# Kernel tuning notes

Hardware: AMD Instinct MI355X
Metric: run time of the kernel (lower is better)

Reference implementation:

```python
import jax, jax.numpy as jnp
import numpy as np

NUM_HEADS = 16

def setup_inputs() -> dict:
    key = jax.random.key(0)
    ks = jax.random.split(key, 8)
    T, B, E = 2048, 2, 1024
    s = 1.0 / np.sqrt(E)
    return {
        "query": jax.random.normal(ks[0], (T, B, E), jnp.float32),
        "key": jax.random.normal(ks[1], (T, B, E), jnp.float32),
        "value": jax.random.normal(ks[2], (T, B, E), jnp.float32),
        "Wq": jax.random.normal(ks[3], (E, E), jnp.float32) * s,
        "bq": jnp.zeros((E,), jnp.float32),
        "Wk": jax.random.normal(ks[4], (E, E), jnp.float32) * s,
        "bk": jnp.zeros((E,), jnp.float32),
        "Wv": jax.random.normal(ks[5], (E, E), jnp.float32) * s,
        "bv": jnp.zeros((E,), jnp.float32),
        "Wo": jax.random.normal(ks[6], (E, E), jnp.float32) * s,
        "bo": jnp.zeros((E,), jnp.float32),
    }

def reference(query, key, value, Wq, bq, Wk, bk, Wv, bv, Wo, bo):
    T, B, E = query.shape
    S = key.shape[0]
    H = NUM_HEADS
    hd = E // H
    scaling = float(hd) ** -0.5
    # linear projections (torch Linear: x @ W.T + b)
    q = (query @ Wq.T + bq).reshape(T, B, H, hd)
    k = (key @ Wk.T + bk).reshape(S, B, H, hd)
    v = (value @ Wv.T + bv).reshape(S, B, H, hd)
    # scores: (B, H, T, S)
    scores = jnp.einsum('tbhd,sbhd->bhts', q, k) * scaling
    attn = jax.nn.softmax(scores, axis=-1)  # dropout p=0
    # weighted sum: (T, B, H, hd) -> (T, B, E)
    out = jnp.einsum('bhts,sbhd->tbhd', attn, v).reshape(T, B, E)
    out = out @ Wo.T + bo
    # averaged attention weights over heads: (B, T, S)
    avg_w = attn.mean(axis=1)
    return (out, avg_w)
```

## Files before the change

### kernel.cpp

```cpp
#include <hip/hip_runtime.h>
#include <hip/hip_bf16.h>
#include <stdint.h>

#define HN 16
#define TT 2048
#define BBATCH 2
#define EE 1024
#define HD 64
#define MM 4096

typedef __attribute__((ext_vector_type(8))) __bf16 bfrag;
typedef __attribute__((ext_vector_type(4))) float f32x4;

__device__ __forceinline__ void gll16(const void* g, void* lds) {
  __builtin_amdgcn_global_load_lds(
      (const __attribute__((address_space(1))) void*)g,
      (__attribute__((address_space(3))) void*)lds, 16, 0, 0);
}

__device__ __forceinline__ f32x4 mfma_bf16(bfrag a, bfrag b, f32x4 c) {
  return __builtin_amdgcn_mfma_f32_16x16x32_bf16(a, b, c, 0, 0, 0);
}

__device__ __forceinline__ const bfrag* fragp(const __bf16* base, int row, int e) {
  return (const bfrag*)(base + row * 64 + ((((e >> 3) ^ row) & 7) << 3));
}
__device__ __forceinline__ int swze(int row, int col) {
  return row * 64 + ((((col >> 3) ^ row) & 7) << 3) + (col & 7);
}
__device__ __forceinline__ void stage8(const __bf16* grow0, int gstride,
                                       __bf16* tile, int r0, int lane) {
  const int rr = lane >> 3;
  const int cl = (lane & 7) ^ rr;
  gll16(grow0 + (size_t)(r0 + rr) * gstride + cl * 8, tile + r0 * 64);
}

struct CvtArgs {
  const float* src[7];
  __bf16* dst[7];
  int n4[7];
};

__global__ __launch_bounds__(256) void cvt_all(CvtArgs a) {
  const int z = blockIdx.z;
  const int i = blockIdx.x * 256 + threadIdx.x;
  if (i < a.n4[z]) {
    float4 v = ((const float4*)a.src[z])[i];
    struct alignas(8) B4 { __bf16 a0, a1, a2, a3; };
    B4 o = {(__bf16)v.x, (__bf16)v.y, (__bf16)v.z, (__bf16)v.w};
    ((B4*)a.dst[z])[i] = o;
  }
}

__device__ __forceinline__ void gemm_core(const __bf16* __restrict__ X,
                                          const __bf16* __restrict__ W,
                                          const float* __restrict__ bias,
                                          void* __restrict__ out, int mode) {
  __shared__ __bf16 As[128 * 32];
  __shared__ __bf16 Bs[128 * 32];
  const int tid = threadIdx.x;
  const int lane = tid & 63, wave = tid >> 6;
  const int wm = wave >> 1, wn = wave & 1;
  const int quad = lane >> 4, l16 = lane & 15;
  const int m0 = blockIdx.y * 128, n0 = blockIdx.x * 128;
  const int srow = lane >> 2;
  const int scol = (lane & 3) * 8;
  const int c0 = 2 * wave;

  f32x4 acc[4][4] = {};

  for (int k0 = 0; k0 < EE; k0 += 32) {
    #pragma unroll
    for (int c = 0; c < 2; ++c) {
      const int ch = c0 + c;
      gll16(X + (size_t)(m0 + ch * 16 + srow) * EE + k0 + scol, As + ch * 512);
      gll16(W + (size_t)(n0 + ch * 16 + srow) * EE + k0 + scol, Bs + ch * 512);
    }
    __syncthreads();
    bfrag a[4], b[4];
    #pragma unroll
    for (int f = 0; f < 4; ++f)
      a[f] = *(const bfrag*)(As + (wm * 64 + f * 16 + l16) * 32 + quad * 8);
    #pragma unroll
    for (int f = 0; f < 4; ++f)
      b[f] = *(const bfrag*)(Bs + (wn * 64 + f * 16 + l16) * 32 + quad * 8);
    #pragma unroll
    for (int fm = 0; fm < 4; ++fm)
      #pragma unroll
      for (int fn = 0; fn < 4; ++fn)
        acc[fm][fn] = mfma_bf16(a[fm], b[fn], acc[fm][fn]);
    __syncthreads();
  }

  float bv[4];
  #pragma unroll
  for (int fn = 0; fn < 4; ++fn) bv[fn] = bias[n0 + wn * 64 + fn * 16 + l16];

  #pragma unroll
  for (int fm = 0; fm < 4; ++fm) {
    #pragma unroll
    for (int r = 0; r < 4; ++r) {
      const int gm = m0 + wm * 64 + fm * 16 + quad * 4 + r;
      #pragma unroll
      for (int fn = 0; fn < 4; ++fn) {
        const int gn = n0 + wn * 64 + fn * 16 + l16;
        const float v = acc[fm][fn][r] + bv[fn];
        if (mode == 0) {
          const int t = gm >> 1, bb = gm & 1, h = gn >> 6, d = gn & 63;
          ((__bf16*)out)[(((size_t)(bb * HN + h)) * TT + t) * HD + d] = (__bf16)v;
        } else {
          const int s = gm >> 1, bb = gm & 1, h = gn >> 6, d = gn & 63;
          ((__bf16*)out)[(((size_t)(bb * HN + h)) * HD + d) * TT + s] = (__bf16)v;
        }
      }
    }
  }
}

__global__ __launch_bounds__(256) void gemm_qkv(
    const __bf16* __restrict__ xq, const __bf16* __restrict__ xk,
    const __bf16* __restrict__ xv, const __bf16* __restrict__ wq,
    const __bf16* __restrict__ wk, const __bf16* __restrict__ wv,
    const float* __restrict__ bq, const float* __restrict__ bk,
    const float* __restrict__ bv, __bf16* __restrict__ qo,
    __bf16* __restrict__ ko, __bf16* __restrict__ vo) {
  const __bf16 *X, *W;
  const float* bias;
  __bf16* out;
  int mode;
  if (blockIdx.z == 0)      { X = xq; W = wq; bias = bq; out = qo; mode = 0; }
  else if (blockIdx.z == 1) { X = xk; W = wk; bias = bk; out = ko; mode = 0; }
  else                      { X = xv; W = wv; bias = bv; out = vo; mode = 2; }
  gemm_core(X, W, bias, out, mode);
}

__global__ __launch_bounds__(256) void gemm_o64(const __bf16* __restrict__ X,
                                                const __bf16* __restrict__ W,
                                                const float* __restrict__ bias,
                                                float* __restrict__ out) {
  __shared__ __bf16 As[64 * 32];
  __shared__ __bf16 Bs[128 * 32];
  const int tid = threadIdx.x;
  const int lane = tid & 63, wave = tid >> 6;
  const int quad = lane >> 4, l16 = lane & 15;
  const int m0 = blockIdx.y * 64, n0 = blockIdx.x * 128;
  const int srow = lane >> 2, scol = (lane & 3) * 8;

  f32x4 acc[4][2] = {};

  for (int k0 = 0; k0 < EE; k0 += 32) {
    gll16(X + (size_t)(m0 + wave * 16 + srow) * EE + k0 + scol, As + wave * 512);
    #pragma unroll
    for (int c = 0; c < 2; ++c) {
      const int ch = 2 * wave + c;
      gll16(W + (size_t)(n0 + ch * 16 + srow) * EE + k0 + scol, Bs + ch * 512);
    }
    __syncthreads();
    bfrag a[4], b2[2];
    #pragma unroll
    for (int f = 0; f < 4; ++f)
      a[f] = *(const bfrag*)(As + (f * 16 + l16) * 32 + quad * 8);
    #pragma unroll
    for (int f = 0; f < 2; ++f)
      b2[f] = *(const bfrag*)(Bs + (wave * 32 + f * 16 + l16) * 32 + quad * 8);
    #pragma unroll
    for (int fm = 0; fm < 4; ++fm)
      #pragma unroll
      for (int fn = 0; fn < 2; ++fn)
        acc[fm][fn] = mfma_bf16(a[fm], b2[fn], acc[fm][fn]);
    __syncthreads();
  }

  float bv[2];
  #pragma unroll
  for (int fn = 0; fn < 2; ++fn) bv[fn] = bias[n0 + wave * 32 + fn * 16 + l16];

  #pragma unroll
  for (int fm = 0; fm < 4; ++fm)
    #pragma unroll
    for (int r = 0; r < 4; ++r) {
      const int gm = m0 + fm * 16 + quad * 4 + r;
      #pragma unroll
      for (int fn = 0; fn < 2; ++fn) {
        const int gn = n0 + wave * 32 + fn * 16 + l16;
        out[(size_t)gm * EE + gn] = acc[fm][fn][r] + bv[fn];
      }
    }
}

__global__ __launch_bounds__(256) void attn_fwd(const __bf16* __restrict__ qb,
                                                const __bf16* __restrict__ kb,
                                                const __bf16* __restrict__ vtb,
                                                __bf16* __restrict__ ob,
                                                float* __restrict__ linv_ws) {
  __shared__ __bf16 QP[128 * 64];
  __shared__ __bf16 Ks[2][64 * 64];
  __shared__ __bf16 Vs[2][64 * 64];

  const int tid = threadIdx.x, lane = tid & 63, w = tid >> 6;
  const int quad = lane >> 4, l16 = lane & 15;
  const int t0 = blockIdx.x * 128;
  const int h = blockIdx.y, b = blockIdx.z;
  const size_t bh = (size_t)(b * HN + h);

  const __bf16* qbase = qb + (bh * TT + t0) * HD;
  const __bf16* kbase = kb + bh * TT * HD;
  const __bf16* vbase = vtb + bh * HD * TT;

  #pragma unroll
  for (int c = 0; c < 4; ++c) stage8(qbase, HD, QP, w * 32 + c * 8, lane);
  #pragma unroll
  for (int c = 0; c < 2; ++c) {
    stage8(kbase, HD, Ks[0], w * 16 + c * 8, lane);
    stage8(vbase + 0, TT, Vs[0], w * 16 + c * 8, lane);
  }
  __syncthreads();

  bfrag qf[2][2];
  #pragma unroll
  for (int f = 0; f < 2; ++f)
    #pragma unroll
    for (int ks = 0; ks < 2; ++ks)
      qf[f][ks] = *fragp(QP, w * 32 + f * 16 + l16, ks * 32 + quad * 8);

  f32x4 oacc[2][4] = {};
  float lpart[2][4] = {};

  for (int it = 0; it < TT / 64; ++it) {
    const int cur = it & 1;
    if (it) __syncthreads();
    if (it + 1 < TT / 64) {
      const int s1 = (it + 1) * 64;
      #pragma unroll
      for (int c = 0; c < 2; ++c) {
        stage8(kbase + (size_t)s1 * HD, HD, Ks[1 - cur], w * 16 + c * 8, lane);
        stage8(vbase + s1, TT, Vs[1 - cur], w * 16 + c * 8, lane);
      }
    }

    f32x4 sacc[2][4] = {};
    #pragma unroll
    for (int ks = 0; ks < 2; ++ks) {
      bfrag kf[4];
      #pragma unroll
      for (int fn = 0; fn < 4; ++fn)
        kf[fn] = *fragp(Ks[cur], fn * 16 + l16, ks * 32 + quad * 8);
      #pragma unroll
      for (int fm = 0; fm < 2; ++fm)
        #pragma unroll
        for (int fn = 0; fn < 4; ++fn)
          sacc[fm][fn] = mfma_bf16(qf[fm][ks], kf[fn], sacc[fm][fn]);
    }

    #pragma unroll
    for (int fm = 0; fm < 2; ++fm)
      #pragma unroll
      for (int fn = 0; fn < 4; ++fn)
        #pragma unroll
        for (int r = 0; r < 4; ++r) {
          const float p = __expf(sacc[fm][fn][r] * 0.125f);
          lpart[fm][r] += p;
          QP[swze(w * 32 + fm * 16 + quad * 4 + r, fn * 16 + l16)] = (__bf16)p;
        }

    #pragma unroll
    for (int ks = 0; ks < 2; ++ks) {
      bfrag pf[2], vf[4];
      #pragma unroll
      for (int fm = 0; fm < 2; ++fm)
        pf[fm] = *fragp(QP, w * 32 + fm * 16 + l16, ks * 32 + quad * 8);
      #pragma unroll
      for (int fn = 0; fn < 4; ++fn)
        vf[fn] = *fragp(Vs[cur], fn * 16 + l16, ks * 32 + quad * 8);
      #pragma unroll
      for (int fm = 0; fm < 2; ++fm)
        #pragma unroll
        for (int fn = 0; fn < 4; ++fn)
          oacc[fm][fn] = mfma_bf16(pf[fm], vf[fn], oacc[fm][fn]);
    }
  }

  float linvv[2][4];
  #pragma unroll
  for (int fm = 0; fm < 2; ++fm)
    #pragma unroll
    for (int r = 0; r < 4; ++r) {
      float v = lpart[fm][r];
      v += __shfl_xor(v, 1, 16);
      v += __shfl_xor(v, 2, 16);
      v += __shfl_xor(v, 4, 16);
      v += __shfl_xor(v, 8, 16);
      linvv[fm][r] = 1.0f / v;
    }
  if (l16 == 0) {
    #pragma unroll
    for (int fm = 0; fm < 2; ++fm)
      #pragma unroll
      for (int r = 0; r < 4; ++r)
        linv_ws[bh * TT + t0 + w * 32 + fm * 16 + quad * 4 + r] = linvv[fm][r];
  }

  #pragma unroll
  for (int fm = 0; fm < 2; ++fm)
    #pragma unroll
    for (int r = 0; r < 4; ++r) {
      const int row = w * 32 + fm * 16 + quad * 4 + r;
      #pragma unroll
      for (int fn = 0; fn < 4; ++fn) {
        const int d = fn * 16 + l16;
        ob[((size_t)(t0 + row) * BBATCH + b) * EE + h * HD + d] =
            (__bf16)(oacc[fm][fn][r] * linvv[fm][r]);
      }
    }
}

__global__ __launch_bounds__(256) void avg_attn(const __bf16* __restrict__ qb,
                                                const __bf16* __restrict__ kb,
                                                const float* __restrict__ linv_ws,
                                                float* __restrict__ avg_out) {
  __shared__ __bf16 Qs[2][128 * 64];
  __shared__ __bf16 Ks2[2][64 * 64];

  const int tid = threadIdx.x, lane = tid & 63, w = tid >> 6;
  const int quad = lane >> 4, l16 = lane & 15;
  const int s0 = blockIdx.x * 64, t0 = blockIdx.y * 128;
  const int b = blockIdx.z;

  {
    const size_t bh0 = (size_t)b * HN;
    #pragma unroll
    for (int c = 0; c < 4; ++c)
      stage8(qb + (bh0 * TT + t0) * HD, HD, Qs[0], w * 32 + c * 8, lane);
    #pragma unroll
    for (int c = 0; c < 2; ++c)
      stage8(kb + (bh0 * TT + s0) * HD, HD, Ks2[0], w * 16 + c * 8, lane);
  }

  f32x4 aacc[2][4] = {};

  for (int h = 0; h < HN; ++h) {
    const int cur = h & 1;
    const size_t bh = (size_t)(b * HN + h);
    __syncthreads();
    if (h + 1 < HN) {
      const size_t bh1 = bh + 1;
      #pragma unroll
      for (int c = 0; c < 4; ++c)
        stage8(qb + (bh1 * TT + t0) * HD, HD, Qs[1 - cur], w * 32 + c * 8, lane);
      #pragma unroll
      for (int c = 0; c < 2; ++c)
        stage8(kb + (bh1 * TT + s0) * HD, HD, Ks2[1 - cur], w * 16 + c * 8, lane);
    }

    f32x4 sacc[2][4] = {};
    #pragma unroll
    for (int ks = 0; ks < 2; ++ks) {
      bfrag qf[2], kf[4];
      #pragma unroll
      for (int fm = 0; fm < 2; ++fm)
        qf[fm] = *fragp(Qs[cur], w * 32 + fm * 16 + l16, ks * 32 + quad * 8);
      #pragma unroll
      for (int fn = 0; fn < 4; ++fn)
        kf[fn] = *fragp(Ks2[cur], fn * 16 + l16, ks * 32 + quad * 8);
      #pragma unroll
      for (int fm = 0; fm < 2; ++fm)
        #pragma unroll
        for (int fn = 0; fn < 4; ++fn)
          sacc[fm][fn] = mfma_bf16(qf[fm], kf[fn], sacc[fm][fn]);
    }

    float lv[2][4];
    #pragma unroll
    for (int fm = 0; fm < 2; ++fm)
      #pragma unroll
      for (int r = 0; r < 4; ++r)
        lv[fm][r] = linv_ws[bh * TT + t0 + w * 32 + fm * 16 + quad * 4 + r];

    #pragma unroll
    for (int fm = 0; fm < 2; ++fm)
      #pragma unroll
      for (int fn = 0; fn < 4; ++fn)
        #pragma unroll
        for (int r = 0; r < 4; ++r)
          aacc[fm][fn][r] += __expf(sacc[fm][fn][r] * 0.125f) * lv[fm][r];
  }

  const float invh = 1.0f / (float)HN;
  #pragma unroll
  for (int fm = 0; fm < 2; ++fm)
    #pragma unroll
    for (int r = 0; r < 4; ++r) {
      const int t = t0 + w * 32 + fm * 16 + quad * 4 + r;
      #pragma unroll
      for (int fn = 0; fn < 4; ++fn) {
        const int s = s0 + fn * 16 + l16;
        avg_out[((size_t)b * TT + t) * TT + s] = aacc[fm][fn][r] * invh;
      }
    }
}

extern "C" void kernel_launch(void* const* d_in, const int* in_sizes, int n_in,
                              void* d_out, int out_size, void* d_ws, size_t ws_size,
                              hipStream_t stream) {
  (void)in_sizes; (void)n_in; (void)out_size; (void)ws_size;
  const float* query = (const float*)d_in[0];
  const float* key   = (const float*)d_in[1];
  const float* value = (const float*)d_in[2];
  const float* Wq = (const float*)d_in[3];
  const float* bq = (const float*)d_in[4];
  const float* Wk = (const float*)d_in[5];
  const float* bk = (const float*)d_in[6];
  const float* Wv = (const float*)d_in[7];
  const float* bv = (const float*)d_in[8];
  const float* Wo = (const float*)d_in[9];
  const float* bo = (const float*)d_in[10];

  char* ws = (char*)d_ws;
  size_t off = 0;
  auto wsalloc = [&](size_t bytes) -> void* {
    void* p = ws + off;
    off += (bytes + 255) & ~(size_t)255;
    return p;
  };
  const size_t XE = (size_t)MM * EE;
  const size_t WE = (size_t)EE * EE;
  __bf16* xq   = (__bf16*)wsalloc(XE * 2);
  __bf16* xk   = (__bf16*)wsalloc(XE * 2);
  __bf16* xv   = (__bf16*)wsalloc(XE * 2);
  __bf16* wqb  = (__bf16*)wsalloc(WE * 2);
  __bf16* wkb  = (__bf16*)wsalloc(WE * 2);
  __bf16* wvb  = (__bf16*)wsalloc(WE * 2);
  __bf16* wob  = (__bf16*)wsalloc(WE * 2);
  __bf16* qbuf = (__bf16*)wsalloc(XE * 2);
  __bf16* kbuf = (__bf16*)wsalloc(XE * 2);
  __bf16* vtbuf= (__bf16*)wsalloc(XE * 2);
  __bf16* obuf = (__bf16*)wsalloc(XE * 2);
  float* linv  = (float*)wsalloc((size_t)BBATCH * HN * TT * 4);

  CvtArgs ca;
  ca.src[0] = query; ca.dst[0] = xq;  ca.n4[0] = (int)(XE / 4);
  ca.src[1] = key;   ca.dst[1] = xk;  ca.n4[1] = (int)(XE / 4);
  ca.src[2] = value; ca.dst[2] = xv;  ca.n4[2] = (int)(XE / 4);
  ca.src[3] = Wq;    ca.dst[3] = wqb; ca.n4[3] = (int)(WE / 4);
  ca.src[4] = Wk;    ca.dst[4] = wkb; ca.n4[4] = (int)(WE / 4);
  ca.src[5] = Wv;    ca.dst[5] = wvb; ca.n4[5] = (int)(WE / 4);
  ca.src[6] = Wo;    ca.dst[6] = wob; ca.n4[6] = (int)(WE / 4);
  cvt_all<<<dim3(4096, 1, 7), 256, 0, stream>>>(ca);

  gemm_qkv<<<dim3(8, 32, 3), 256, 0, stream>>>(xq, xk, xv, wqb, wkb, wvb,
                                               bq, bk, bv, qbuf, kbuf, vtbuf);

  attn_fwd<<<dim3(16, HN, BBATCH), 256, 0, stream>>>(qbuf, kbuf, vtbuf, obuf, linv);

  float* avg_out = (float*)d_out + (size_t)TT * BBATCH * EE;
  avg_attn<<<dim3(32, 16, 2), 256, 0, stream>>>(qbuf, kbuf, linv, avg_out);

  gemm_o64<<<dim3(8, 64), 256, 0, stream>>>(obuf, wob, bo, (float*)d_out);
}
```

Measured before the change: 300.4 us.

## Use 2-wave blocks with 64-row wave tiles and transposed S=K·Q softmax in attention

Attention and averaged-weights kernels now launch 128 threads, and each wave handles 64 query rows instead of 32, doubling the MFMA work per wave and the reuse of loaded K/V fragments. In attn_fwd the score MFMA is transposed to K·Q, so each lane owns a query row. This lets the row sum be reduced with two shuffles and lets P be written to LDS as packed 4-element bf16 stores. avg_attn loads the per-row inverse sums as vectors. The larger register tiles may raise VGPR pressure, and the 512-block grids have half as many waves, which may lower occupancy.

```diff
diff --git a/kernel.cpp b/kernel.cpp
--- a/kernel.cpp
+++ b/kernel.cpp
@@ -24,9 +24,6 @@
 
 __device__ __forceinline__ const bfrag* fragp(const __bf16* base, int row, int e) {
   return (const bfrag*)(base + row * 64 + ((((e >> 3) ^ row) & 7) << 3));
-}
-__device__ __forceinline__ int swze(int row, int col) {
-  return row * 64 + ((((col >> 3) ^ row) & 7) << 3) + (col & 7);
 }
 __device__ __forceinline__ void stage8(const __bf16* grow0, int gstride,
                                        __bf16* tile, int r0, int lane) {
@@ -188,7 +185,7 @@
     }
 }
 
-__global__ __launch_bounds__(256) void attn_fwd(const __bf16* __restrict__ qb,
+__global__ __launch_bounds__(128) void attn_fwd(const __bf16* __restrict__ qb,
                                                 const __bf16* __restrict__ kb,
                                                 const __bf16* __restrict__ vtb,
                                                 __bf16* __restrict__ ob,
@@ -196,6 +193,7 @@
   __shared__ __bf16 QP[128 * 64];
   __shared__ __bf16 Ks[2][64 * 64];
   __shared__ __bf16 Vs[2][64 * 64];
+  __shared__ float LinvS[128];
 
   const int tid = threadIdx.x, lane = tid & 63, w = tid >> 6;
   const int quad = lane >> 4, l16 = lane & 15;
@@ -208,23 +206,23 @@
   const __bf16* vbase = vtb + bh * HD * TT;
 
   #pragma unroll
-  for (int c = 0; c < 4; ++c) stage8(qbase, HD, QP, w * 32 + c * 8, lane);
-  #pragma unroll
-  for (int c = 0; c < 2; ++c) {
-    stage8(kbase, HD, Ks[0], w * 16 + c * 8, lane);
-    stage8(vbase + 0, TT, Vs[0], w * 16 + c * 8, lane);
+  for (int c = 0; c < 8; ++c) stage8(qbase, HD, QP, w * 64 + c * 8, lane);
+  #pragma unroll
+  for (int c = 0; c < 4; ++c) {
+    stage8(kbase, HD, Ks[0], w * 32 + c * 8, lane);
+    stage8(vbase, TT, Vs[0], w * 32 + c * 8, lane);
   }
   __syncthreads();
 
-  bfrag qf[2][2];
-  #pragma unroll
-  for (int f = 0; f < 2; ++f)
+  bfrag qf[4][2];
+  #pragma unroll
+  for (int fn = 0; fn < 4; ++fn)
     #pragma unroll
     for (int ks = 0; ks < 2; ++ks)
-      qf[f][ks] = *fragp(QP, w * 32 + f * 16 + l16, ks * 32 + quad * 8);
-
-  f32x4 oacc[2][4] = {};
-  float lpart[2][4] = {};
+      qf[fn][ks] = *fragp(QP, w * 64 + fn * 16 + l16, ks * 32 + quad * 8);
+
+  f32x4 oacc[4][4] = {};
+  float lpart[4] = {};
 
   for (int it = 0; it < TT / 64; ++it) {
     const int cur = it & 1;
@@ -232,89 +230,90 @@
     if (it + 1 < TT / 64) {
       const int s1 = (it + 1) * 64;
       #pragma unroll
-      for (int c = 0; c < 2; ++c) {
-        stage8(kbase + (size_t)s1 * HD, HD, Ks[1 - cur], w * 16 + c * 8, lane);
-        stage8(vbase + s1, TT, Vs[1 - cur], w * 16 + c * 8, lane);
-      }
-    }
-
-    f32x4 sacc[2][4] = {};
+      for (int c = 0; c < 4; ++c) {
+        stage8(kbase + (size_t)s1 * HD, HD, Ks[1 - cur], w * 32 + c * 8, lane);
+        stage8(vbase + s1, TT, Vs[1 - cur], w * 32 + c * 8, lane);
+      }
+    }
+
+    f32x4 sacc[4][4] = {};
     #pragma unroll
     for (int ks = 0; ks < 2; ++ks) {
       bfrag kf[4];
       #pragma unroll
-      for (int fn = 0; fn < 4; ++fn)
-        kf[fn] = *fragp(Ks[cur], fn * 16 + l16, ks * 32 + quad * 8);
-      #pragma unroll
-      for (int fm = 0; fm < 2; ++fm)
+      for (int f = 0; f < 4; ++f)
+        kf[f] = *fragp(Ks[cur], f * 16 + l16, ks * 32 + quad * 8);
+      #pragma unroll
+      for (int fm = 0; fm < 4; ++fm)
         #pragma unroll
         for (int fn = 0; fn < 4; ++fn)
-          sacc[fm][fn] = mfma_bf16(qf[fm][ks], kf[fn], sacc[fm][fn]);
-    }
-
-    #pragma unroll
-    for (int fm = 0; fm < 2; ++fm)
-      #pragma unroll
-      for (int fn = 0; fn < 4; ++fn)
-        #pragma unroll
-        for (int r = 0; r < 4; ++r) {
-          const float p = __expf(sacc[fm][fn][r] * 0.125f);
-          lpart[fm][r] += p;
-          QP[swze(w * 32 + fm * 16 + quad * 4 + r, fn * 16 + l16)] = (__bf16)p;
-        }
+          sacc[fm][fn] = mfma_bf16(kf[fm], qf[fn][ks], sacc[fm][fn]);
+    }
+
+    #pragma unroll
+    for (int fn = 0; fn < 4; ++fn) {
+      const int row = w * 64 + fn * 16 + l16;
+      float acc_l = 0.0f;
+      #pragma unroll
+      for (int fm = 0; fm < 4; ++fm) {
+        float p0 = __expf(sacc[fm][fn][0] * 0.125f);
+        float p1 = __expf(sacc[fm][fn][1] * 0.125f);
+        float p2 = __expf(sacc[fm][fn][2] * 0.125f);
+        float p3 = __expf(sacc[fm][fn][3] * 0.125f);
+        acc_l += (p0 + p1) + (p2 + p3);
+        struct alignas(8) B4 { __bf16 v0, v1, v2, v3; };
+        B4 pk = {(__bf16)p0, (__bf16)p1, (__bf16)p2, (__bf16)p3};
+        const int chunk = (fm * 2 + (quad >> 1)) ^ (row & 7);
+        *(B4*)(QP + row * 64 + chunk * 8 + (quad & 1) * 4) = pk;
+      }
+      lpart[fn] += acc_l;
+    }
 
     #pragma unroll
     for (int ks = 0; ks < 2; ++ks) {
-      bfrag pf[2], vf[4];
-      #pragma unroll
-      for (int fm = 0; fm < 2; ++fm)
-        pf[fm] = *fragp(QP, w * 32 + fm * 16 + l16, ks * 32 + quad * 8);
-      #pragma unroll
-      for (int fn = 0; fn < 4; ++fn)
-        vf[fn] = *fragp(Vs[cur], fn * 16 + l16, ks * 32 + quad * 8);
-      #pragma unroll
-      for (int fm = 0; fm < 2; ++fm)
+      bfrag pf[4], vf[4];
+      #pragma unroll
+      for (int f = 0; f < 4; ++f)
+        pf[f] = *fragp(QP, w * 64 + f * 16 + l16, ks * 32 + quad * 8);
+      #pragma unroll
+      for (int f = 0; f < 4; ++f)
+        vf[f] = *fragp(Vs[cur], f * 16 + l16, ks * 32 + quad * 8);
+      #pragma unroll
+      for (int fm = 0; fm < 4; ++fm)
         #pragma unroll
         for (int fn = 0; fn < 4; ++fn)
           oacc[fm][fn] = mfma_bf16(pf[fm], vf[fn], oacc[fm][fn]);
     }
   }
 
-  float linvv[2][4];
-  #pragma unroll
-  for (int fm = 0; fm < 2; ++fm)
+  #pragma unroll
+  for (int fn = 0; fn < 4; ++fn) {
+    float v = lpart[fn];
+    v += __shfl_xor(v, 16);
+    v += __shfl_xor(v, 32);
+    const float linv = 1.0f / v;
+    if (quad == 0) {
+      LinvS[w * 64 + fn * 16 + l16] = linv;
+      linv_ws[bh * TT + t0 + w * 64 + fn * 16 + l16] = linv;
+    }
+  }
+  #pragma unroll
+  for (int fm = 0; fm < 4; ++fm) {
+    const f32x4 lv = *(const f32x4*)&LinvS[w * 64 + fm * 16 + quad * 4];
     #pragma unroll
     for (int r = 0; r < 4; ++r) {
-      float v = lpart[fm][r];
-      v += __shfl_xor(v, 1, 16);
-      v += __shfl_xor(v, 2, 16);
-      v += __shfl_xor(v, 4, 16);
-      v += __shfl_xor(v, 8, 16);
-      linvv[fm][r] = 1.0f / v;
-    }
-  if (l16 == 0) {
-    #pragma unroll
-    for (int fm = 0; fm < 2; ++fm)
-      #pragma unroll
-      for (int r = 0; r < 4; ++r)
-        linv_ws[bh * TT + t0 + w * 32 + fm * 16 + quad * 4 + r] = linvv[fm][r];
-  }
-
-  #pragma unroll
-  for (int fm = 0; fm < 2; ++fm)
-    #pragma unroll
-    for (int r = 0; r < 4; ++r) {
-      const int row = w * 32 + fm * 16 + quad * 4 + r;
+      const int row = w * 64 + fm * 16 + quad * 4 + r;
       #pragma unroll
       for (int fn = 0; fn < 4; ++fn) {
         const int d = fn * 16 + l16;
         ob[((size_t)(t0 + row) * BBATCH + b) * EE + h * HD + d] =
-            (__bf16)(oacc[fm][fn][r] * linvv[fm][r]);
-      }
-    }
-}
-
-__global__ __launch_bounds__(256) void avg_attn(const __bf16* __restrict__ qb,
+            (__bf16)(oacc[fm][fn][r] * lv[r]);
+      }
+    }
+  }
+}
+
+__global__ __launch_bounds__(128) void avg_attn(const __bf16* __restrict__ qb,
                                                 const __bf16* __restrict__ kb,
                                                 const float* __restrict__ linv_ws,
                                                 float* __restrict__ avg_out) {
@@ -329,14 +328,14 @@
   {
     const size_t bh0 = (size_t)b * HN;
     #pragma unroll
+    for (int c = 0; c < 8; ++c)
+      stage8(qb + (bh0 * TT + t0) * HD, HD, Qs[0], w * 64 + c * 8, lane);
+    #pragma unroll
     for (int c = 0; c < 4; ++c)
-      stage8(qb + (bh0 * TT + t0) * HD, HD, Qs[0], w * 32 + c * 8, lane);
-    #pragma unroll
-    for (int c = 0; c < 2; ++c)
-      stage8(kb + (bh0 * TT + s0) * HD, HD, Ks2[0], w * 16 + c * 8, lane);
-  }
-
-  f32x4 aacc[2][4] = {};
+      stage8(kb + (bh0 * TT + s0) * HD, HD, Ks2[0], w * 32 + c * 8, lane);
+  }
+
+  f32x4 aacc[4][4] = {};
 
   for (int h = 0; h < HN; ++h) {
     const int cur = h & 1;
@@ -345,52 +344,50 @@
     if (h + 1 < HN) {
       const size_t bh1 = bh + 1;
       #pragma unroll
+      for (int c = 0; c < 8; ++c)
+        stage8(qb + (bh1 * TT + t0) * HD, HD, Qs[1 - cur], w * 64 + c * 8, lane);
+      #pragma unroll
       for (int c = 0; c < 4; ++c)
-        stage8(qb + (bh1 * TT + t0) * HD, HD, Qs[1 - cur], w * 32 + c * 8, lane);
-      #pragma unroll
-      for (int c = 0; c < 2; ++c)
-        stage8(kb + (bh1 * TT + s0) * HD, HD, Ks2[1 - cur], w * 16 + c * 8, lane);
-    }
-
-    f32x4 sacc[2][4] = {};
+        stage8(kb + (bh1 * TT + s0) * HD, HD, Ks2[1 - cur], w * 32 + c * 8, lane);
+    }
+
+    f32x4 sacc[4][4] = {};
     #pragma unroll
     for (int ks = 0; ks < 2; ++ks) {
-      bfrag qf[2], kf[4];
-      #pragma unroll
-      for (int fm = 0; fm < 2; ++fm)
-        qf[fm] = *fragp(Qs[cur], w * 32 + fm * 16 + l16, ks * 32 + quad * 8);
-      #pragma unroll
-      for (int fn = 0; fn < 4; ++fn)
-        kf[fn] = *fragp(Ks2[cur], fn * 16 + l16, ks * 32 + quad * 8);
-      #pragma unroll
-      for (int fm = 0; fm < 2; ++fm)
+      bfrag qf4[4], kf4[4];
+      #pragma unroll
+      for (int f = 0; f < 4; ++f)
+        qf4[f] = *fragp(Qs[cur], w * 64 + f * 16 + l16, ks * 32 + quad * 8);
+      #pragma unroll
+      for (int f = 0; f < 4; ++f)
+        kf4[f] = *fragp(Ks2[cur], f * 16 + l16, ks * 32 + quad * 8);
+      #pragma unroll
+      for (int fm = 0; fm < 4; ++fm)
         #pragma unroll
         for (int fn = 0; fn < 4; ++fn)
-          sacc[fm][fn] = mfma_bf16(qf[fm], kf[fn], sacc[fm][fn]);
-    }
-
-    float lv[2][4];
-    #pragma unroll
-    for (int fm = 0; fm < 2; ++fm)
-      #pragma unroll
-      for (int r = 0; r < 4; ++r)
-        lv[fm][r] = linv_ws[bh * TT + t0 + w * 32 + fm * 16 + quad * 4 + r];
-
-    #pragma unroll
-    for (int fm = 0; fm < 2; ++fm)
+          sacc[fm][fn] = mfma_bf16(qf4[fm], kf4[fn], sacc[fm][fn]);
+    }
+
+    f32x4 lvv[4];
+    #pragma unroll
+    for (int fm = 0; fm < 4; ++fm)
+      lvv[fm] = *(const f32x4*)&linv_ws[bh * TT + t0 + w * 64 + fm * 16 + quad * 4];
+
+    #pragma unroll
+    for (int fm = 0; fm < 4; ++fm)
       #pragma unroll
       for (int fn = 0; fn < 4; ++fn)
         #pragma unroll
         for (int r = 0; r < 4; ++r)
-          aacc[fm][fn][r] += __expf(sacc[fm][fn][r] * 0.125f) * lv[fm][r];
+          aacc[fm][fn][r] += __expf(sacc[fm][fn][r] * 0.125f) * lvv[fm][r];
   }
 
   const float invh = 1.0f / (float)HN;
   #pragma unroll
-  for (int fm = 0; fm < 2; ++fm)
+  for (int fm = 0; fm < 4; ++fm)
     #pragma unroll
     for (int r = 0; r < 4; ++r) {
-      const int t = t0 + w * 32 + fm * 16 + quad * 4 + r;
+      const int t = t0 + w * 64 + fm * 16 + quad * 4 + r;
       #pragma unroll
       for (int fn = 0; fn < 4; ++fn) {
         const int s = s0 + fn * 16 + l16;
@@ -450,10 +447,10 @@
   gemm_qkv<<<dim3(8, 32, 3), 256, 0, stream>>>(xq, xk, xv, wqb, wkb, wvb,
                                                bq, bk, bv, qbuf, kbuf, vtbuf);
 
-  attn_fwd<<<dim3(16, HN, BBATCH), 256, 0, stream>>>(qbuf, kbuf, vtbuf, obuf, linv);
+  attn_fwd<<<dim3(16, HN, BBATCH), 128, 0, stream>>>(qbuf, kbuf, vtbuf, obuf, linv);
 
   float* avg_out = (float*)d_out + (size_t)TT * BBATCH * EE;
-  avg_attn<<<dim3(32, 16, 2), 256, 0, stream>>>(qbuf, kbuf, linv, avg_out);
+  avg_attn<<<dim3(32, 16, 2), 128, 0, stream>>>(qbuf, kbuf, linv, avg_out);
 
   gemm_o64<<<dim3(8, 64), 256, 0, stream>>>(obuf, wob, bo, (float*)d_out);
 }
```

Measured after the change: 317.3 us. +5.6%, slower.
